# Kernel tuning notes

Hardware: AMD Instinct MI355X
Metric: run time of the kernel (lower is better)

Reference implementation:

```python
import jax, jax.numpy as jnp
import numpy as np

NUM_EMBEDDINGS = 8192
EMBEDDING_DIM = 512
COMMITMENT_COST = 0.25


def setup_inputs() -> dict:
    key = jax.random.key(0)
    kx, ke = jax.random.split(key)
    x = jax.random.normal(kx, (32, 512, 512), dtype=jnp.float32)
    # codebook ~ uniform init as in nn.Embedding default-ish; scale is arbitrary for a reference
    codebook = jax.random.normal(ke, (NUM_EMBEDDINGS, EMBEDDING_DIM), dtype=jnp.float32)
    return {"x": x, "codebook": codebook}


def reference(x, codebook):
    # x: [B, T, D], codebook: [K, D]
    input_shape = x.shape
    flat = x.reshape(-1, EMBEDDING_DIM)                     # [N, D]
    x2 = jnp.sum(flat * flat, axis=1, keepdims=True)        # [N, 1]
    e2 = jnp.sum(codebook * codebook, axis=1)               # [K]
    dists = x2 + e2 - 2.0 * jnp.matmul(flat, codebook.T)    # [N, K]
    encoding_indices = jnp.argmin(dists, axis=1)            # [N] int
    min_distances = jnp.min(dists, axis=1)                  # [N]
    quantized = codebook[encoding_indices].reshape(input_shape)  # [B, T, D]
    # straight-through estimator
    quantized_st = x + jax.lax.stop_gradient(quantized - x)
    # losses (sum reduction, matching F.mse_loss(..., reduction='sum'))
    loss_vq = jnp.sum((quantized - jax.lax.stop_gradient(x)) ** 2)
    loss_commit = jnp.sum((x - jax.lax.stop_gradient(quantized)) ** 2)
    # use_ema = False -> loss includes codebook term
    loss = loss_commit * COMMITMENT_COST + loss_vq
    encoding_indices = encoding_indices.reshape(input_shape[:-1])
    min_distances = min_distances.reshape(input_shape[:-1])
    return quantized_st, loss, encoding_indices, min_distances, loss_commit
```

## Files before the change

kernel.cpp:

```cpp
#include <hip/hip_runtime.h>
#include <hip/hip_bf16.h>
#include <math.h>

#define NUM_EMB 8192
#define DIM 512
#define NROWS 16384
#define NPART 4096

typedef unsigned short ushort;
typedef unsigned long long ull;
typedef __attribute__((ext_vector_type(8))) short short8;
typedef __attribute__((ext_vector_type(4))) float floatx4;

__device__ __forceinline__ ushort f2bf(float f) {
    unsigned u = __float_as_uint(f);
    unsigned r = (u + 0x7fffu + ((u >> 16) & 1u)) >> 16;
    return (ushort)r;
}
__device__ __forceinline__ float bf2f(ushort h) {
    return __uint_as_float(((unsigned)h) << 16);
}
__device__ __forceinline__ unsigned fmap(float f) {
    unsigned u = __float_as_uint(f);
    return (u & 0x80000000u) ? ~u : (u | 0x80000000u);
}
__device__ __forceinline__ float funmap(unsigned m) {
    return __uint_as_float((m & 0x80000000u) ? (m ^ 0x80000000u) : ~m);
}
__device__ __forceinline__ void gld16(const void* g, void* l) {
    __builtin_amdgcn_global_load_lds(
        (const __attribute__((address_space(1))) void*)g,
        (__attribute__((address_space(3))) void*)l, 16, 0, 0);
}

__global__ __launch_bounds__(256) void split_rss_k(const float* __restrict__ src,
    ushort* __restrict__ hi, ushort* __restrict__ lo, float* __restrict__ ss, int nrows)
{
    int gid  = blockIdx.x * blockDim.x + threadIdx.x;
    int row  = gid >> 6;
    int lane = threadIdx.x & 63;
    if (row >= nrows) return;
    const float4* r = (const float4*)(src + (size_t)row * DIM);
    ushort4* h4 = (ushort4*)(hi + (size_t)row * DIM);
    ushort4* l4 = (ushort4*)(lo + (size_t)row * DIM);
    float s = 0.f;
#pragma unroll
    for (int i = lane; i < DIM / 4; i += 64) {
        float4 v = r[i];
        s += v.x * v.x + v.y * v.y + v.z * v.z + v.w * v.w;
        ushort4 h, l;
        h.x = f2bf(v.x); l.x = f2bf(v.x - bf2f(h.x));
        h.y = f2bf(v.y); l.y = f2bf(v.y - bf2f(h.y));
        h.z = f2bf(v.z); l.z = f2bf(v.z - bf2f(h.z));
        h.w = f2bf(v.w); l.w = f2bf(v.w - bf2f(h.w));
        h4[i] = h; l4[i] = l;
    }
#pragma unroll
    for (int off = 32; off > 0; off >>= 1) s += __shfl_down(s, off, 64);
    if (lane == 0) ss[row] = s;
}

__global__ __launch_bounds__(256) void init_k(ull* __restrict__ packed)
{
    int i = blockIdx.x * 256 + threadIdx.x;
    if (i < NROWS) packed[i] = ~0ull;
}

__global__ __launch_bounds__(256, 4) void dist_mfma_k(
    const ushort* __restrict__ xh, const ushort* __restrict__ xl,
    const ushort* __restrict__ ch, const ushort* __restrict__ cl,
    const float* __restrict__ e2, ull* __restrict__ packed)
{
    __shared__ ushort Ah[128 * 32];
    __shared__ ushort Al[128 * 32];
    __shared__ ushort Bh[128 * 32];
    __shared__ ushort Bl[128 * 32];

    const int tid  = threadIdx.x;
    const int lane = tid & 63;
    const int w    = tid >> 6;
    const int wm   = w >> 1, wn = w & 1;
    const int row0 = blockIdx.x * 128;
    const int col0 = blockIdx.y * 128;

    floatx4 acc[4][4];
#pragma unroll
    for (int m = 0; m < 4; ++m)
#pragma unroll
        for (int n = 0; n < 4; ++n) acc[m][n] = (floatx4){0.f, 0.f, 0.f, 0.f};

    const int c0 = tid, c1 = tid + 256;
    const int r0c = c0 >> 2, s0c = (c0 & 3) * 8;
    const int r1c = c1 >> 2, s1c = (c1 & 3) * 8;
    const int ga0 = (row0 + r0c) * DIM + s0c;
    const int ga1 = (row0 + r1c) * DIM + s1c;
    const int gb0 = (col0 + r0c) * DIM + s0c;
    const int gb1 = (col0 + r1c) * DIM + s1c;
    const int l0 = c0 * 8, l1 = c1 * 8;

    const int fr = (lane & 15) * 32 + (lane >> 4) * 8;

    for (int kk = 0; kk < 16; ++kk) {
        const int dk = kk * 32;
        __syncthreads();
        gld16(&xh[ga0 + dk], &Ah[l0]);  gld16(&xh[ga1 + dk], &Ah[l1]);
        gld16(&xl[ga0 + dk], &Al[l0]);  gld16(&xl[ga1 + dk], &Al[l1]);
        gld16(&ch[gb0 + dk], &Bh[l0]);  gld16(&ch[gb1 + dk], &Bh[l1]);
        gld16(&cl[gb0 + dk], &Bl[l0]);  gld16(&cl[gb1 + dk], &Bl[l1]);
        __syncthreads();

        short8 ah[4], al[4], bh[4], bl[4];
#pragma unroll
        for (int m = 0; m < 4; ++m) {
            const int o = (wm * 64 + m * 16) * 32 + fr;
            ah[m] = *(const short8*)&Ah[o];
            al[m] = *(const short8*)&Al[o];
        }
#pragma unroll
        for (int n = 0; n < 4; ++n) {
            const int o = (wn * 64 + n * 16) * 32 + fr;
            bh[n] = *(const short8*)&Bh[o];
            bl[n] = *(const short8*)&Bl[o];
        }
#pragma unroll
        for (int m = 0; m < 4; ++m)
#pragma unroll
            for (int n = 0; n < 4; ++n) {
                acc[m][n] = __builtin_amdgcn_mfma_f32_16x16x32_bf16(ah[m], bh[n], acc[m][n], 0, 0, 0);
                acc[m][n] = __builtin_amdgcn_mfma_f32_16x16x32_bf16(ah[m], bl[n], acc[m][n], 0, 0, 0);
                acc[m][n] = __builtin_amdgcn_mfma_f32_16x16x32_bf16(al[m], bh[n], acc[m][n], 0, 0, 0);
            }
    }

    float e2v[4];
    int   cidx[4];
#pragma unroll
    for (int n = 0; n < 4; ++n) {
        cidx[n] = col0 + wn * 64 + n * 16 + (lane & 15);
        e2v[n]  = e2[cidx[n]];
    }
#pragma unroll
    for (int m = 0; m < 4; ++m) {
#pragma unroll
        for (int r = 0; r < 4; ++r) {
            float bv = INFINITY; int bi = 0x7fffffff;
#pragma unroll
            for (int n = 0; n < 4; ++n) {
                float v = e2v[n] - 2.f * acc[m][n][r];
                if (v < bv) { bv = v; bi = cidx[n]; }
            }
#pragma unroll
            for (int mk = 1; mk < 16; mk <<= 1) {
                float ov = __shfl_xor(bv, mk, 64);
                int   oi = __shfl_xor(bi, mk, 64);
                if (ov < bv || (ov == bv && oi < bi)) { bv = ov; bi = oi; }
            }
            if ((lane & 15) == 0) {
                int grow = row0 + wm * 64 + m * 16 + (lane >> 4) * 4 + r;
                ull pack = ((ull)fmap(bv) << 32) | (unsigned)bi;
                atomicMin(&packed[grow], pack);
            }
        }
    }
}

__global__ __launch_bounds__(256) void merge_k(const ull* __restrict__ packed,
    const float* __restrict__ x2, float* __restrict__ out_idx,
    float* __restrict__ out_mind, int* __restrict__ idx_ws)
{
    int row = blockIdx.x * blockDim.x + threadIdx.x;
    if (row >= NROWS) return;
    ull p = packed[row];
    int bi = (int)(p & 0xffffffffull);
    float m = funmap((unsigned)(p >> 32));
    out_idx[row]  = (float)bi;
    out_mind[row] = x2[row] + m;
    idx_ws[row]   = bi;
}

__global__ __launch_bounds__(256) void gather_loss_k(const float* __restrict__ x,
    const float* __restrict__ cb, const int* __restrict__ idx,
    float* __restrict__ outq, float* __restrict__ partials)
{
    __shared__ float ps[4];
    int gid  = blockIdx.x * blockDim.x + threadIdx.x;
    int row  = gid >> 6;
    int lane = threadIdx.x & 63;
    int w    = threadIdx.x >> 6;
    float s = 0.f;
    if (row < NROWS) {
        const int k = idx[row];
        const float4* q  = (const float4*)(cb + (size_t)k * DIM);
        const float4* xr = (const float4*)(x + (size_t)row * DIM);
        float4* o = (float4*)(outq + (size_t)row * DIM);
#pragma unroll
        for (int i = lane; i < DIM / 4; i += 64) {
            float4 qv = q[i], xv = xr[i];
            o[i] = qv;
            float dx = xv.x - qv.x, dy = xv.y - qv.y;
            float dz = xv.z - qv.z, dw = xv.w - qv.w;
            s += dx * dx + dy * dy + dz * dz + dw * dw;
        }
    }
#pragma unroll
    for (int off = 32; off > 0; off >>= 1) s += __shfl_down(s, off, 64);
    if (lane == 0) ps[w] = s;
    __syncthreads();
    if (threadIdx.x == 0) partials[blockIdx.x] = ps[0] + ps[1] + ps[2] + ps[3];
}

__global__ __launch_bounds__(256) void finalize_k(const float* __restrict__ partials,
    float* __restrict__ out_loss, float* __restrict__ out_commit)
{
    __shared__ float ps[4];
    int t = threadIdx.x, lane = t & 63, w = t >> 6;
    float s = 0.f;
#pragma unroll
    for (int i = 0; i < NPART / 256; ++i) s += partials[t + 256 * i];
#pragma unroll
    for (int off = 32; off > 0; off >>= 1) s += __shfl_down(s, off, 64);
    if (lane == 0) ps[w] = s;
    __syncthreads();
    if (t == 0) {
        float tot = ps[0] + ps[1] + ps[2] + ps[3];
        *out_loss   = 0.25f * tot + tot;
        *out_commit = tot;
    }
}

#define BM 64
#define BN 64
#define BK 32
#define KSPLIT 4
#define KPER (NUM_EMB / KSPLIT)
#define NCT (KPER / BN)

__global__ __launch_bounds__(256) void rowsumsq_k(const float* __restrict__ a,
                                                  float* __restrict__ out, int nrows)
{
    int gid  = blockIdx.x * blockDim.x + threadIdx.x;
    int row  = gid >> 6;
    int lane = threadIdx.x & 63;
    if (row >= nrows) return;
    const float4* r = (const float4*)(a + (size_t)row * DIM);
    float s = 0.f;
#pragma unroll
    for (int i = lane; i < DIM / 4; i += 64) {
        float4 v = r[i];
        s += v.x * v.x + v.y * v.y + v.z * v.z + v.w * v.w;
    }
#pragma unroll
    for (int off = 32; off > 0; off >>= 1) s += __shfl_down(s, off, 64);
    if (lane == 0) out[row] = s;
}

__global__ __launch_bounds__(256) void dist_argmin_old_k(const float* __restrict__ x,
    const float* __restrict__ cb, const float* __restrict__ e2,
    float* __restrict__ part_m, int* __restrict__ part_i)
{
    __shared__ __align__(16) float As[BK][BM + 4];
    __shared__ __align__(16) float Bs[BK][BN + 4];
    __shared__ float redv[BM][16];
    __shared__ int   redi[BM][16];

    const int row0 = blockIdx.x * BM;
    const int ks   = blockIdx.y;
    const int cbeg = ks * KPER;
    const int t    = threadIdx.x;
    const int tx   = t & 15;
    const int ty   = t >> 4;
    const int ld_d = t & 31;
    const int ld_r = t >> 5;

    float minm[4]; int mini[4];
#pragma unroll
    for (int i = 0; i < 4; ++i) { minm[i] = INFINITY; mini[i] = 0; }

    for (int ct = 0; ct < NCT; ++ct) {
        const int c0 = cbeg + ct * BN;
        float acc[4][4];
#pragma unroll
        for (int i = 0; i < 4; ++i)
#pragma unroll
            for (int j = 0; j < 4; ++j) acc[i][j] = 0.f;
        for (int dc = 0; dc < DIM; dc += BK) {
#pragma unroll
            for (int rr = 0; rr < BM; rr += 8)
                As[ld_d][ld_r + rr] = x[(size_t)(row0 + ld_r + rr) * DIM + dc + ld_d];
#pragma unroll
            for (int rr = 0; rr < BN; rr += 8)
                Bs[ld_d][ld_r + rr] = cb[(size_t)(c0 + ld_r + rr) * DIM + dc + ld_d];
            __syncthreads();
#pragma unroll
            for (int d = 0; d < BK; ++d) {
                float4 av = *(const float4*)&As[d][4 * ty];
                float4 bv = *(const float4*)&Bs[d][4 * tx];
                acc[0][0] += av.x * bv.x; acc[0][1] += av.x * bv.y;
                acc[0][2] += av.x * bv.z; acc[0][3] += av.x * bv.w;
                acc[1][0] += av.y * bv.x; acc[1][1] += av.y * bv.y;
                acc[1][2] += av.y * bv.z; acc[1][3] += av.y * bv.w;
                acc[2][0] += av.z * bv.x; acc[2][1] += av.z * bv.y;
                acc[2][2] += av.z * bv.z; acc[2][3] += av.z * bv.w;
                acc[3][0] += av.w * bv.x; acc[3][1] += av.w * bv.y;
                acc[3][2] += av.w * bv.z; acc[3][3] += av.w * bv.w;
            }
            __syncthreads();
        }
#pragma unroll
        for (int j = 0; j < 4; ++j) {
            const int c = c0 + 4 * tx + j;
            const float e = e2[c];
#pragma unroll
            for (int i = 0; i < 4; ++i) {
                float m = e - 2.f * acc[i][j];
                if (m < minm[i]) { minm[i] = m; mini[i] = c; }
            }
        }
    }
#pragma unroll
    for (int i = 0; i < 4; ++i) {
        redv[4 * ty + i][tx] = minm[i];
        redi[4 * ty + i][tx] = mini[i];
    }
    __syncthreads();
    if (t < BM) {
        float bm = INFINITY; int bi = 0;
#pragma unroll
        for (int c = 0; c < 16; ++c) {
            float v = redv[t][c];
            if (v < bm) { bm = v; bi = redi[t][c]; }
        }
        part_m[(size_t)(row0 + t) * KSPLIT + ks] = bm;
        part_i[(size_t)(row0 + t) * KSPLIT + ks] = bi;
    }
}

__global__ __launch_bounds__(256) void merge_old_k(const float* __restrict__ part_m,
    const int* __restrict__ part_i, const float* __restrict__ x2,
    float* __restrict__ out_idx, float* __restrict__ out_mind, int* __restrict__ idx_ws)
{
    int row = blockIdx.x * blockDim.x + threadIdx.x;
    if (row >= NROWS) return;
    float bm = INFINITY; int bi = 0;
#pragma unroll
    for (int s = 0; s < KSPLIT; ++s) {
        float v = part_m[(size_t)row * KSPLIT + s];
        if (v < bm) { bm = v; bi = part_i[(size_t)row * KSPLIT + s]; }
    }
    out_idx[row]  = (float)bi;
    out_mind[row] = x2[row] + bm;
    idx_ws[row]   = bi;
}

extern "C" void kernel_launch(void* const* d_in, const int* in_sizes, int n_in,
                              void* d_out, int out_size, void* d_ws, size_t ws_size,
                              hipStream_t stream)
{
    const float* x  = (const float*)d_in[0];
    const float* cb = (const float*)d_in[1];
    float* out = (float*)d_out;

    float* outq       = out;
    float* out_loss   = out + 8388608;
    float* out_idx    = out + 8388609;
    float* out_mind   = out + 8388609 + 16384;
    float* out_commit = out + 8388609 + 2 * 16384;

    char* ws = (char*)d_ws;
    float* e2      = (float*)ws;   ws += NUM_EMB * 4;
    float* x2      = (float*)ws;   ws += NROWS * 4;
    ull*   packed  = (ull*)ws;     ws += NROWS * 8;
    int*   idxw    = (int*)ws;     ws += NROWS * 4;
    float* partials= (float*)ws;   ws += NPART * 4;
    ushort* xh = (ushort*)ws;      ws += (size_t)NROWS * DIM * 2;
    ushort* xl = (ushort*)ws;      ws += (size_t)NROWS * DIM * 2;
    ushort* ch = (ushort*)ws;      ws += (size_t)NUM_EMB * DIM * 2;
    ushort* cl = (ushort*)ws;      ws += (size_t)NUM_EMB * DIM * 2;
    size_t need_fast = (size_t)(ws - (char*)d_ws);

    if (ws_size >= need_fast) {
        init_k<<<NROWS / 256, 256, 0, stream>>>(packed);
        split_rss_k<<<NROWS / 4, 256, 0, stream>>>(x, xh, xl, x2, NROWS);
        split_rss_k<<<NUM_EMB / 4, 256, 0, stream>>>(cb, ch, cl, e2, NUM_EMB);
        dim3 grid(NROWS / 128, NUM_EMB / 128);
        dist_mfma_k<<<grid, 256, 0, stream>>>(xh, xl, ch, cl, e2, packed);
        merge_k<<<NROWS / 256, 256, 0, stream>>>(packed, x2, out_idx, out_mind, idxw);
    } else {
        rowsumsq_k<<<NUM_EMB / 4, 256, 0, stream>>>(cb, e2, NUM_EMB);
        rowsumsq_k<<<NROWS / 4, 256, 0, stream>>>(x, x2, NROWS);
        float* pm = (float*)((char*)d_ws + NUM_EMB * 4 + NROWS * 4);
        int*   pi = (int*)(pm + (size_t)NROWS * KSPLIT);
        int*   idxw2 = pi + (size_t)NROWS * KSPLIT;
        float* partials2 = (float*)(idxw2 + NROWS);
        idxw = idxw2; partials = partials2;
        dim3 grid(NROWS / BM, KSPLIT);
        dist_argmin_old_k<<<grid, 256, 0, stream>>>(x, cb, e2, pm, pi);
        merge_old_k<<<NROWS / 256, 256, 0, stream>>>(pm, pi, x2, out_idx, out_mind, idxw);
    }

    gather_loss_k<<<NROWS / 4, 256, 0, stream>>>(x, cb, idxw, outq, partials);
    finalize_k<<<1, 256, 0, stream>>>(partials, out_loss, out_commit);
}
```

Before: 494.9 us.

## Swizzle LDS tile layout and fold init/merge kernels into neighbors

XOR-swizzles the 16-byte chunk positions in the shared-memory A/B tiles, applied on both the global-to-LDS load addresses and the MFMA fragment reads, to cut LDS bank conflicts in the distance GEMM. It also removes the separate init and merge kernels. The packed argmin buffer is now reset inside the row-norm split kernel, and the packed result is decoded inside the gather/loss kernel. This saves two launches and one pass over small per-row arrays, and the fallback path is reworked to write the packed format.

```diff
diff --git a/kernel.cpp b/kernel.cpp
--- a/kernel.cpp
+++ b/kernel.cpp
@@ -34,7 +34,8 @@
 }
 
 __global__ __launch_bounds__(256) void split_rss_k(const float* __restrict__ src,
-    ushort* __restrict__ hi, ushort* __restrict__ lo, float* __restrict__ ss, int nrows)
+    ushort* __restrict__ hi, ushort* __restrict__ lo, float* __restrict__ ss,
+    ull* __restrict__ packed, int nrows)
 {
     int gid  = blockIdx.x * blockDim.x + threadIdx.x;
     int row  = gid >> 6;
@@ -57,13 +58,10 @@
     }
 #pragma unroll
     for (int off = 32; off > 0; off >>= 1) s += __shfl_down(s, off, 64);
-    if (lane == 0) ss[row] = s;
-}
-
-__global__ __launch_bounds__(256) void init_k(ull* __restrict__ packed)
-{
-    int i = blockIdx.x * 256 + threadIdx.x;
-    if (i < NROWS) packed[i] = ~0ull;
+    if (lane == 0) {
+        ss[row] = s;
+        if (packed) packed[row] = ~0ull;
+    }
 }
 
 __global__ __launch_bounds__(256, 4) void dist_mfma_k(
@@ -90,15 +88,15 @@
         for (int n = 0; n < 4; ++n) acc[m][n] = (floatx4){0.f, 0.f, 0.f, 0.f};
 
     const int c0 = tid, c1 = tid + 256;
-    const int r0c = c0 >> 2, s0c = (c0 & 3) * 8;
-    const int r1c = c1 >> 2, s1c = (c1 & 3) * 8;
+    const int r0c = c0 >> 2, s0c = (((c0 & 3) ^ ((c0 >> 3) & 3))) * 8;
+    const int r1c = c1 >> 2, s1c = (((c1 & 3) ^ ((c1 >> 3) & 3))) * 8;
     const int ga0 = (row0 + r0c) * DIM + s0c;
     const int ga1 = (row0 + r1c) * DIM + s1c;
     const int gb0 = (col0 + r0c) * DIM + s0c;
     const int gb1 = (col0 + r1c) * DIM + s1c;
     const int l0 = c0 * 8, l1 = c1 * 8;
 
-    const int fr = (lane & 15) * 32 + (lane >> 4) * 8;
+    const int fr = (lane & 15) * 32 + (((lane >> 4) ^ ((lane >> 1) & 3)) * 8);
 
     for (int kk = 0; kk < 16; ++kk) {
         const int dk = kk * 32;
@@ -164,23 +162,11 @@
     }
 }
 
-__global__ __launch_bounds__(256) void merge_k(const ull* __restrict__ packed,
-    const float* __restrict__ x2, float* __restrict__ out_idx,
-    float* __restrict__ out_mind, int* __restrict__ idx_ws)
-{
-    int row = blockIdx.x * blockDim.x + threadIdx.x;
-    if (row >= NROWS) return;
-    ull p = packed[row];
-    int bi = (int)(p & 0xffffffffull);
-    float m = funmap((unsigned)(p >> 32));
-    out_idx[row]  = (float)bi;
-    out_mind[row] = x2[row] + m;
-    idx_ws[row]   = bi;
-}
-
 __global__ __launch_bounds__(256) void gather_loss_k(const float* __restrict__ x,
-    const float* __restrict__ cb, const int* __restrict__ idx,
-    float* __restrict__ outq, float* __restrict__ partials)
+    const float* __restrict__ cb, const ull* __restrict__ packed,
+    const float* __restrict__ x2, float* __restrict__ outq,
+    float* __restrict__ out_idx, float* __restrict__ out_mind,
+    float* __restrict__ partials)
 {
     __shared__ float ps[4];
     int gid  = blockIdx.x * blockDim.x + threadIdx.x;
@@ -189,7 +175,12 @@
     int w    = threadIdx.x >> 6;
     float s = 0.f;
     if (row < NROWS) {
-        const int k = idx[row];
+        ull p = packed[row];
+        int k = (int)(p & 0xffffffffull);
+        if (lane == 0) {
+            out_idx[row]  = (float)k;
+            out_mind[row] = x2[row] + funmap((unsigned)(p >> 32));
+        }
         const float4* q  = (const float4*)(cb + (size_t)k * DIM);
         const float4* xr = (const float4*)(x + (size_t)row * DIM);
         float4* o = (float4*)(outq + (size_t)row * DIM);
@@ -335,9 +326,8 @@
     }
 }
 
-__global__ __launch_bounds__(256) void merge_old_k(const float* __restrict__ part_m,
-    const int* __restrict__ part_i, const float* __restrict__ x2,
-    float* __restrict__ out_idx, float* __restrict__ out_mind, int* __restrict__ idx_ws)
+__global__ __launch_bounds__(256) void merge_pack_k(const float* __restrict__ part_m,
+    const int* __restrict__ part_i, ull* __restrict__ packed)
 {
     int row = blockIdx.x * blockDim.x + threadIdx.x;
     if (row >= NROWS) return;
@@ -347,9 +337,7 @@
         float v = part_m[(size_t)row * KSPLIT + s];
         if (v < bm) { bm = v; bi = part_i[(size_t)row * KSPLIT + s]; }
     }
-    out_idx[row]  = (float)bi;
-    out_mind[row] = x2[row] + bm;
-    idx_ws[row]   = bi;
+    packed[row] = ((ull)fmap(bm) << 32) | (unsigned)bi;
 }
 
 extern "C" void kernel_launch(void* const* d_in, const int* in_sizes, int n_in,
@@ -370,7 +358,6 @@
     float* e2      = (float*)ws;   ws += NUM_EMB * 4;
     float* x2      = (float*)ws;   ws += NROWS * 4;
     ull*   packed  = (ull*)ws;     ws += NROWS * 8;
-    int*   idxw    = (int*)ws;     ws += NROWS * 4;
     float* partials= (float*)ws;   ws += NPART * 4;
     ushort* xh = (ushort*)ws;      ws += (size_t)NROWS * DIM * 2;
     ushort* xl = (ushort*)ws;      ws += (size_t)NROWS * DIM * 2;
@@ -379,25 +366,21 @@
     size_t need_fast = (size_t)(ws - (char*)d_ws);
 
     if (ws_size >= need_fast) {
-        init_k<<<NROWS / 256, 256, 0, stream>>>(packed);
-        split_rss_k<<<NROWS / 4, 256, 0, stream>>>(x, xh, xl, x2, NROWS);
-        split_rss_k<<<NUM_EMB / 4, 256, 0, stream>>>(cb, ch, cl, e2, NUM_EMB);
+        split_rss_k<<<NROWS / 4, 256, 0, stream>>>(x, xh, xl, x2, packed, NROWS);
+        split_rss_k<<<NUM_EMB / 4, 256, 0, stream>>>(cb, ch, cl, e2, (ull*)0, NUM_EMB);
         dim3 grid(NROWS / 128, NUM_EMB / 128);
         dist_mfma_k<<<grid, 256, 0, stream>>>(xh, xl, ch, cl, e2, packed);
-        merge_k<<<NROWS / 256, 256, 0, stream>>>(packed, x2, out_idx, out_mind, idxw);
     } else {
         rowsumsq_k<<<NUM_EMB / 4, 256, 0, stream>>>(cb, e2, NUM_EMB);
         rowsumsq_k<<<NROWS / 4, 256, 0, stream>>>(x, x2, NROWS);
-        float* pm = (float*)((char*)d_ws + NUM_EMB * 4 + NROWS * 4);
+        float* pm = (float*)((char*)d_ws + NUM_EMB * 4 + NROWS * 4 + NROWS * 8 + NPART * 4);
         int*   pi = (int*)(pm + (size_t)NROWS * KSPLIT);
-        int*   idxw2 = pi + (size_t)NROWS * KSPLIT;
-        float* partials2 = (float*)(idxw2 + NROWS);
-        idxw = idxw2; partials = partials2;
         dim3 grid(NROWS / BM, KSPLIT);
         dist_argmin_old_k<<<grid, 256, 0, stream>>>(x, cb, e2, pm, pi);
-        merge_old_k<<<NROWS / 256, 256, 0, stream>>>(pm, pi, x2, out_idx, out_mind, idxw);
-    }
-
-    gather_loss_k<<<NROWS / 4, 256, 0, stream>>>(x, cb, idxw, outq, partials);
+        merge_pack_k<<<NROWS / 256, 256, 0, stream>>>(pm, pi, packed);
+    }
+
+    gather_loss_k<<<NROWS / 4, 256, 0, stream>>>(x, cb, packed, x2, outq,
+                                                 out_idx, out_mind, partials);
     finalize_k<<<1, 256, 0, stream>>>(partials, out_loss, out_commit);
 }
```

New measurement: 483.2 us. 2.4% less time.
